# Kernel optimization log

Hardware: AMD Instinct MI355X
Metric: run time of the kernel (lower is better)

Reference implementation:

```python
import jax, jax.numpy as jnp
import numpy as np

H, L, N = 512, 2048, 64  # channels, seq len, SSM state size


def _make_dplr_hippo(n):
    # make_HiPPO / make_NPLR_HiPPO / make_DPLR_HiPPO from the source
    p0 = np.sqrt(1.0 + 2.0 * np.arange(n))
    A = p0[:, None] * p0[None, :]
    A = np.tril(A) - np.diag(np.arange(n))
    nhippo = -A
    P = np.sqrt(np.arange(n) + 0.5)
    B = np.sqrt(2.0 * np.arange(n) + 1.0)
    S = nhippo + P[:, None] * P[None, :]
    S_diag = np.diagonal(S)
    Lam_re = np.mean(S_diag) * np.ones_like(S_diag)
    Lam_im, V = jnp.linalg.eigh(jnp.asarray(S, jnp.complex64) * (-1j))
    Pc = V.conj().T @ jnp.asarray(P, jnp.complex64)
    Bc = V.conj().T @ jnp.asarray(B, jnp.complex64)
    return (jnp.asarray(Lam_re, jnp.float32), jnp.asarray(Lam_im, jnp.float32),
            Pc, Bc)


def setup_inputs() -> dict:
    key = jax.random.key(0)
    k_u, k_c, k_s = jax.random.split(key, 3)
    Lre, Lim, Pc, Bc = _make_dplr_hippo(N)
    tile = lambda v: jnp.tile(v[None, :], (H, 1)).astype(jnp.float32)  # (H,N)
    return {
        "u": jax.random.normal(k_u, (L, H), dtype=jnp.float32),
        "x0_re": jnp.zeros((N, H), jnp.float32),
        "x0_im": jnp.zeros((N, H), jnp.float32),
        "Lambda_re": tile(Lre),
        "Lambda_im": tile(Lim),
        "P_re": tile(Pc.real), "P_im": tile(Pc.imag),
        "B_re": tile(Bc.real), "B_im": tile(Bc.imag),
        "C": jax.random.normal(k_c, (H, N, 2), jnp.float32) * (0.5 ** 0.5),
        "D": jnp.ones((H, 1), jnp.float32),
        "log_step": jax.random.uniform(k_s, (H, 1), jnp.float32,
                                       minval=np.log(1e-3), maxval=np.log(1e-1)),
    }


def _discretize(Lam, P, B, Ct, step):
    # discrete_DPLR with Q = P (as in setup); per-channel, vmapped over H.
    n = Lam.shape[0]
    I = jnp.eye(n, dtype=jnp.complex64)
    A = jnp.diag(Lam) - P[:, None] * P.conj()[None, :]
    A0 = (2.0 / step) * I + A
    Dd = jnp.diag(1.0 / (2.0 / step - Lam))
    Qc = P.conj()[None, :]            # (1,N)
    P2 = P[:, None]                   # (N,1)
    A1 = Dd - (Dd @ P2) * (1.0 / (1.0 + Qc @ Dd @ P2)) * (Qc @ Dd)
    Ab = A1 @ A0                      # (N,N)
    Bb = 2.0 * (A1 @ B[:, None])[:, 0]
    AbL = jnp.linalg.matrix_power(Ab, L)
    Cb = (Ct[None, :] @ jnp.linalg.inv(I - AbL).conj()).conj()[0]
    return Ab, Bb, Cb


def _forward(u, x0_re, x0_im, Lambda_re, Lambda_im, P_re, P_im,
             B_re, B_im, C, D, log_step):
    Lam = jnp.clip(Lambda_re, None, -0.0001) + 1j * Lambda_im  # (H,N)
    Pc = P_re + 1j * P_im
    Bc = B_re + 1j * B_im
    Cc = C[..., 0] + 1j * C[..., 1]
    step = jnp.exp(log_step)[:, 0]                              # (H,)
    Ab, Bb, Cb = jax.vmap(_discretize)(Lam, Pc, Bc, Cc, step)   # (H,N,N),(H,N),(H,N)

    x0 = jnp.transpose(x0_re + 1j * x0_im)                      # (H,N) complex

    def body(x, u_t):  # x: (H,N) complex, u_t: (H,)
        x = jnp.einsum('hnm,hm->hn', Ab, x) + Bb * u_t[:, None]
        y = jnp.einsum('hn,hn->h', Cb, x)
        return x, y.real

    _, ys = jax.lax.scan(body, x0, u)                           # ys: (L,H)
    return ys + u * D[:, 0][None, :]                            # (L,H) float32


def reference(u, x0_re, x0_im, Lambda_re, Lambda_im, P_re, P_im,
              B_re, B_im, C, D, log_step):
    return _forward(u, x0_re, x0_im, Lambda_re, Lambda_im, P_re, P_im,
                    B_re, B_im, C, D, log_step)
```

## Files before the change

kernel.cpp:

```cpp
#include <hip/hip_runtime.h>

#define HH 512
#define LL 2048
#define NN 64
#define TT 64
#define CC 32
#define NLDA 68
#define SP 72

typedef __attribute__((ext_vector_type(8))) short bf16x8_t;
typedef __attribute__((ext_vector_type(4))) float floatx4;

__device__ __forceinline__ float2 cmul(float2 a, float2 b) {
    return make_float2(a.x * b.x - a.y * b.y, a.x * b.y + a.y * b.x);
}
__device__ __forceinline__ float2 crecip(float2 a) {
    float id = 1.0f / (a.x * a.x + a.y * a.y);
    return make_float2(a.x * id, -a.y * id);
}
template <int CTRL>
__device__ __forceinline__ float dpp_mov(float x) {
    return __int_as_float(__builtin_amdgcn_update_dpp(
        0, __float_as_int(x), CTRL, 0xf, 0xf, true));
}
__device__ __forceinline__ float wave_sum_bcast(float x) {
    x += dpp_mov<0x111>(x);
    x += dpp_mov<0x112>(x);
    x += dpp_mov<0x114>(x);
    x += dpp_mov<0x118>(x);
    x += dpp_mov<0x142>(x);
    x += dpp_mov<0x143>(x);
    return __int_as_float(__builtin_amdgcn_readlane(__float_as_int(x), 63));
}
__device__ __forceinline__ float rlane(float x, int i) {
    return __int_as_float(__builtin_amdgcn_readlane(__float_as_int(x), i));
}
__device__ __forceinline__ unsigned short f2bf(float f) {
    unsigned int u = __float_as_uint(f);
    u += 0x7FFFu + ((u >> 16) & 1u);
    return (unsigned short)(u >> 16);
}
__device__ __forceinline__ float bf2f(unsigned short s) {
    return __uint_as_float(((unsigned int)s) << 16);
}

__device__ __forceinline__ void closed_form(
    int h, int n,
    const float* __restrict__ Lre, const float* __restrict__ Lim,
    const float* __restrict__ Pre, const float* __restrict__ Pim,
    const float* __restrict__ Bre, const float* __restrict__ Bim,
    const float* __restrict__ logstep,
    float2& da, float2& DPv, float2& tv, float2& bb) {
    float step = expf(logstep[h]);
    float as = 2.0f / step;
    float lr = fminf(Lre[h * NN + n], -1e-4f);
    float li = Lim[h * NN + n];
    float2 a = make_float2(as + lr, li);
    float2 Dn = crecip(make_float2(as - lr, -li));
    float2 P = make_float2(Pre[h * NN + n], Pim[h * NN + n]);
    float2 Bv = make_float2(Bre[h * NN + n], Bim[h * NN + n]);
    float2 cP = make_float2(P.x, -P.y);
    float p2 = P.x * P.x + P.y * P.y;
    float2 rt = cmul(cmul(cP, Dn), Bv);
    float2 e = make_float2(wave_sum_bcast(Dn.x * p2), wave_sum_bcast(Dn.y * p2));
    float2 rv = make_float2(wave_sum_bcast(rt.x), wave_sum_bcast(rt.y));
    float2 cc = crecip(make_float2(1.0f + e.x, e.y));
    da = cmul(Dn, a);
    DPv = cmul(Dn, P);
    float2 tmp = cmul(cc, make_float2(da.x - e.x, da.y - e.y));
    tv = cmul(cP, make_float2(1.0f + tmp.x, tmp.y));
    float2 crv = cmul(cc, rv);
    float2 cd = cmul(crv, DPv);
    float2 db = cmul(Dn, Bv);
    bb = make_float2(2.0f * (db.x - cd.x), 2.0f * (db.y - cd.y));
}

__device__ __forceinline__ void pack_tiles(
    unsigned short* mRh, unsigned short* mRl,
    unsigned short* mIh, unsigned short* mIl,
    unsigned short* mTRh, unsigned short* mTRl,
    unsigned short* mTIh, unsigned short* mTIl,
    int w, int lm, int q, const float Cr[4][4], const float Ci[4][4]) {
    #pragma unroll
    for (int nt = 0; nt < 4; ++nt) {
        const int c = nt * 16 + lm;
        unsigned short hr[4], lr_[4], hi_[4], li_[4];
        #pragma unroll
        for (int reg = 0; reg < 4; ++reg) {
            const float xr = Cr[nt][reg], xi = Ci[nt][reg];
            hr[reg] = f2bf(xr); lr_[reg] = f2bf(xr - bf2f(hr[reg]));
            hi_[reg] = f2bf(xi); li_[reg] = f2bf(xi - bf2f(hi_[reg]));
            const int r = 16 * w + 4 * q + reg;
            mRh[r * SP + c] = hr[reg]; mRl[r * SP + c] = lr_[reg];
            mIh[r * SP + c] = hi_[reg]; mIl[r * SP + c] = li_[reg];
        }
        const int tb = c * SP + 16 * w + 4 * q;
        *(ushort4*)&mTRh[tb] = make_ushort4(hr[0], hr[1], hr[2], hr[3]);
        *(ushort4*)&mTRl[tb] = make_ushort4(lr_[0], lr_[1], lr_[2], lr_[3]);
        *(ushort4*)&mTIh[tb] = make_ushort4(hi_[0], hi_[1], hi_[2], hi_[3]);
        *(ushort4*)&mTIl[tb] = make_ushort4(li_[0], li_[1], li_[2], li_[3]);
    }
}

extern "C" __global__ void __launch_bounds__(256, 2)
k_fusedA(const float* __restrict__ Lre, const float* __restrict__ Lim,
         const float* __restrict__ Pre, const float* __restrict__ Pim,
         const float* __restrict__ Bre, const float* __restrict__ Bim,
         const float* __restrict__ Cmat, const float* __restrict__ logstep,
         const float* __restrict__ u,
         float2* __restrict__ wM, float2* __restrict__ wCb,
         float2* __restrict__ wP) {
    extern __shared__ __align__(16) char smem[];
    const int tid = threadIdx.x;

    if (blockIdx.x < HH) {
        const int h = blockIdx.x;
        unsigned short* mRh  = (unsigned short*)smem;
        unsigned short* mRl  = mRh + 64 * SP;
        unsigned short* mIh  = mRl + 64 * SP;
        unsigned short* mIl  = mIh + 64 * SP;
        unsigned short* mTRh = mIl + 64 * SP;
        unsigned short* mTRl = mTRh + 64 * SP;
        unsigned short* mTIh = mTRl + 64 * SP;
        unsigned short* mTIl = mTIh + 64 * SP;
        float* Nr = (float*)smem;
        float* Ni = Nr + 64 * NLDA;
        float2* sda  = (float2*)(smem + 73728);
        float2* sDP  = sda + NN;
        float2* st   = sDP + NN;
        float2* sBb  = st + NN;
        float2* srhs = sBb + NN;
        float2* sx   = srhs + NN;
        float2* pp   = sx + NN;

        const int w = tid >> 6;
        const int lane = tid & 63;
        const int lm = lane & 15, q = lane >> 4;

        if (tid < NN) {
            float2 da, DPv, tv, bb;
            closed_form(h, tid, Lre, Lim, Pre, Pim, Bre, Bim, logstep,
                        da, DPv, tv, bb);
            sda[tid] = da; sDP[tid] = DPv; st[tid] = tv; sBb[tid] = bb;
            srhs[tid] = make_float2(Cmat[h * NN * 2 + tid * 2],
                                    -Cmat[h * NN * 2 + tid * 2 + 1]);
        }
        __syncthreads();

        {
            float Cr[4][4], Ci[4][4];
            #pragma unroll
            for (int nt = 0; nt < 4; ++nt) {
                const int c = nt * 16 + lm;
                const float2 tc = st[c];
                #pragma unroll
                for (int reg = 0; reg < 4; ++reg) {
                    const int r = 16 * w + 4 * q + reg;
                    const float2 dp = sDP[r];
                    float vr = -(dp.x * tc.x - dp.y * tc.y);
                    float vi = -(dp.x * tc.y + dp.y * tc.x);
                    if (r == c) { vr += sda[r].x; vi += sda[r].y; }
                    Cr[nt][reg] = vr; Ci[nt][reg] = vi;
                }
            }
            pack_tiles(mRh, mRl, mIh, mIl, mTRh, mTRl, mTIh, mTIl,
                       w, lm, q, Cr, Ci);
        }
        __syncthreads();

        const int arow = (16 * w + lm) * SP + q * 8;
        for (int it = 0; it < 11; ++it) {
            floatx4 z4 = {0.f, 0.f, 0.f, 0.f};
            floatx4 aP[4] = {z4, z4, z4, z4};
            floatx4 aQ[4] = {z4, z4, z4, z4};
            floatx4 aC[4] = {z4, z4, z4, z4};
            for (int k2 = 0; k2 < 2; ++k2) {
                const int ao = arow + k2 * 32;
                const bf16x8_t ARh = *(const bf16x8_t*)&mRh[ao];
                const bf16x8_t ARl = *(const bf16x8_t*)&mRl[ao];
                const bf16x8_t AIh = *(const bf16x8_t*)&mIh[ao];
                const bf16x8_t AIl = *(const bf16x8_t*)&mIl[ao];
                bf16x8_t BRh[4], BRl[4], BIh[4], BIl[4];
                #pragma unroll
                for (int nt = 0; nt < 4; ++nt) {
                    const int bo = (nt * 16 + lm) * SP + k2 * 32 + q * 8;
                    BRh[nt] = *(const bf16x8_t*)&mTRh[bo];
                    BRl[nt] = *(const bf16x8_t*)&mTRl[bo];
                    BIh[nt] = *(const bf16x8_t*)&mTIh[bo];
                    BIl[nt] = *(const bf16x8_t*)&mTIl[bo];
                }
                #pragma unroll
                for (int nt = 0; nt < 4; ++nt) {
                    aP[nt] = __builtin_amdgcn_mfma_f32_16x16x32_bf16(ARh, BRh[nt], aP[nt], 0, 0, 0);
                    aP[nt] = __builtin_amdgcn_mfma_f32_16x16x32_bf16(ARh, BRl[nt], aP[nt], 0, 0, 0);
                    aP[nt] = __builtin_amdgcn_mfma_f32_16x16x32_bf16(ARl, BRh[nt], aP[nt], 0, 0, 0);
                    aQ[nt] = __builtin_amdgcn_mfma_f32_16x16x32_bf16(AIh, BIh[nt], aQ[nt], 0, 0, 0);
                    aQ[nt] = __builtin_amdgcn_mfma_f32_16x16x32_bf16(AIh, BIl[nt], aQ[nt], 0, 0, 0);
                    aQ[nt] = __builtin_amdgcn_mfma_f32_16x16x32_bf16(AIl, BIh[nt], aQ[nt], 0, 0, 0);
                    aC[nt] = __builtin_amdgcn_mfma_f32_16x16x32_bf16(ARh, BIh[nt], aC[nt], 0, 0, 0);
                    aC[nt] = __builtin_amdgcn_mfma_f32_16x16x32_bf16(ARh, BIl[nt], aC[nt], 0, 0, 0);
                    aC[nt] = __builtin_amdgcn_mfma_f32_16x16x32_bf16(ARl, BIh[nt], aC[nt], 0, 0, 0);
                    aC[nt] = __builtin_amdgcn_mfma_f32_16x16x32_bf16(AIh, BRh[nt], aC[nt], 0, 0, 0);
                    aC[nt] = __builtin_amdgcn_mfma_f32_16x16x32_bf16(AIh, BRl[nt], aC[nt], 0, 0, 0);
                    aC[nt] = __builtin_amdgcn_mfma_f32_16x16x32_bf16(AIl, BRh[nt], aC[nt], 0, 0, 0);
                }
            }
            __syncthreads();
            if (it < 10) {
                float Cr[4][4], Ci[4][4];
                #pragma unroll
                for (int nt = 0; nt < 4; ++nt)
                    #pragma unroll
                    for (int reg = 0; reg < 4; ++reg) {
                        Cr[nt][reg] = aP[nt][reg] - aQ[nt][reg];
                        Ci[nt][reg] = aC[nt][reg];
                    }
                pack_tiles(mRh, mRl, mIh, mIl, mTRh, mTRl, mTIh, mTIl,
                           w, lm, q, Cr, Ci);
                __syncthreads();
                if (it == 5) {
                    for (int idx = tid; idx < NN * NN; idx += 256) {
                        const int c = idx >> 6, k = idx & 63;
                        wM[h * NN * NN + idx] = make_float2(
                            bf2f(mTRh[c * SP + k]) + bf2f(mTRl[c * SP + k]),
                            bf2f(mTIh[c * SP + k]) + bf2f(mTIl[c * SP + k]));
                    }
                }
            } else {
                #pragma unroll
                for (int nt = 0; nt < 4; ++nt) {
                    const int c = nt * 16 + lm;
                    #pragma unroll
                    for (int reg = 0; reg < 4; ++reg) {
                        const int r = 16 * w + 4 * q + reg;
                        Nr[r * NLDA + c] = aP[nt][reg] - aQ[nt][reg];
                        Ni[r * NLDA + c] = aC[nt][reg];
                    }
                }
                __syncthreads();
            }
        }

        if (tid < NN) sx[tid] = srhs[tid];
        __syncthreads();
        for (int itn = 0; itn < 24; ++itn) {
            const int i = tid & 63, qq = tid >> 6;
            float pr = 0.0f, pi = 0.0f;
            #pragma unroll 4
            for (int jj = 0; jj < 16; ++jj) {
                const int j = qq * 16 + jj;
                const float nr = Nr[j * NLDA + i], ni = Ni[j * NLDA + i];
                const float2 xj = sx[j];
                pr += nr * xj.x - ni * xj.y;
                pi += nr * xj.y + ni * xj.x;
            }
            pp[qq * 64 + i] = make_float2(pr, pi);
            __syncthreads();
            if (tid < NN) {
                const float2 a0 = pp[tid], a1 = pp[64 + tid];
                const float2 a2 = pp[128 + tid], a3 = pp[192 + tid];
                sx[tid] = make_float2(
                    srhs[tid].x + a0.x + a1.x + a2.x + a3.x,
                    srhs[tid].y + a0.y + a1.y + a2.y + a3.y);
            }
            __syncthreads();
        }
        if (tid < NN) wCb[h * NN + tid] = sx[tid];
    } else {
        const int h = blockIdx.x - HH;
        float2* sG  = (float2*)smem;
        float*  su  = (float*)(smem + 32768);
        float2* sda = (float2*)(smem + 40960);
        float2* sDP = sda + NN;
        float2* st  = sDP + NN;
        float2* sBb = st + NN;

        const int wv = tid >> 6, lane = tid & 63;
        for (int idx = tid; idx < LL; idx += 256)
            su[idx] = u[idx * HH + h];
        if (tid < NN) {
            float2 da, DPv, tv, bb;
            closed_form(h, tid, Lre, Lim, Pre, Pim, Bre, Bim, logstep,
                        da, DPv, tv, bb);
            sda[tid] = da; sDP[tid] = DPv; st[tid] = tv; sBb[tid] = bb;
        }
        __syncthreads();

        if (tid < 64) {
            const float2 da = sda[lane], DP = sDP[lane], tt = st[lane];
            float Gr = sBb[lane].x, Gi = sBb[lane].y;
            for (int m = 0; m < TT; ++m) {
                sG[m * NN + lane] = make_float2(Gr, Gi);
                float c1 = tt.x * Gr - tt.y * Gi;
                float c2 = tt.x * Gi + tt.y * Gr;
                c1 += dpp_mov<0x111>(c1); c2 += dpp_mov<0x111>(c2);
                c1 += dpp_mov<0x112>(c1); c2 += dpp_mov<0x112>(c2);
                c1 += dpp_mov<0x114>(c1); c2 += dpp_mov<0x114>(c2);
                c1 += dpp_mov<0x118>(c1); c2 += dpp_mov<0x118>(c2);
                c1 += dpp_mov<0x142>(c1); c2 += dpp_mov<0x142>(c2);
                c1 += dpp_mov<0x143>(c1); c2 += dpp_mov<0x143>(c2);
                const float S1 = rlane(c1, 63);
                const float S2 = rlane(c2, 63);
                float nGr = da.x * Gr - da.y * Gi - (DP.x * S1 - DP.y * S2);
                float nGi = da.x * Gi + da.y * Gr - (DP.x * S2 + DP.y * S1);
                Gr = nGr; Gi = nGi;
            }
        }
        __syncthreads();

        float accr[8] = {}, acci[8] = {};
        for (int j = 0; j < TT; ++j) {
            const float2 g = sG[(TT - 1 - j) * NN + lane];
            #pragma unroll
            for (int qc = 0; qc < 8; ++qc) {
                const float uv = su[((wv * 8 + qc) << 6) + j];
                accr[qc] += g.x * uv; acci[qc] += g.y * uv;
            }
        }
        #pragma unroll
        for (int qc = 0; qc < 8; ++qc)
            wP[(h * CC + wv * 8 + qc) * NN + lane] = make_float2(accr[qc], acci[qc]);
    }
}

extern "C" __global__ void __launch_bounds__(256, 2)
k_fusedB(const float* __restrict__ Lre, const float* __restrict__ Lim,
         const float* __restrict__ Pre, const float* __restrict__ Pim,
         const float* __restrict__ Bre, const float* __restrict__ Bim,
         const float* __restrict__ logstep,
         const float* __restrict__ u, const float* __restrict__ Dvec,
         const float* __restrict__ x0_re, const float* __restrict__ x0_im,
         const float2* __restrict__ wM, const float2* __restrict__ wCb,
         const float2* __restrict__ wP, float* __restrict__ out) {
    extern __shared__ __align__(16) char smem[];
    float2* sM          = (float2*)smem;
    unsigned short* sVr = (unsigned short*)(smem + 32768);
    unsigned short* sVi = (unsigned short*)(smem + 41216);
    float2* sXs         = (float2*)(smem + 49664);
    float*  su          = (float*)(smem + 66048);
    float*  sK          = (float*)(smem + 74240);

    const int h = blockIdx.x;
    const int tid = threadIdx.x;
    const int wv = tid >> 6, lane = tid & 63;

    for (int idx = tid; idx < NN * NN; idx += 256)
        sM[idx] = wM[h * NN * NN + idx];
    for (int idx = tid; idx < LL; idx += 256)
        su[idx] = u[idx * HH + h];
    __syncthreads();

    if (wv == 0) {
        float2 da, DP, tt, Bb;
        closed_form(h, lane, Lre, Lim, Pre, Pim, Bre, Bim, logstep,
                    da, DP, tt, Bb);
        const float2 Cb = wCb[h * NN + lane];
        float Gr = Bb.x, Gi = Bb.y;
        float vr = Cb.x, vi = Cb.y;
        for (int m = 0; m < TT; ++m) {
            float ch[5];
            ch[0] = Cb.x * Gr - Cb.y * Gi;
            ch[1] = tt.x * Gr - tt.y * Gi;
            ch[2] = tt.x * Gi + tt.y * Gr;
            ch[3] = vr * DP.x - vi * DP.y;
            ch[4] = vr * DP.y + vi * DP.x;
            #pragma unroll
            for (int c = 0; c < 5; ++c) ch[c] += dpp_mov<0x111>(ch[c]);
            #pragma unroll
            for (int c = 0; c < 5; ++c) ch[c] += dpp_mov<0x112>(ch[c]);
            #pragma unroll
            for (int c = 0; c < 5; ++c) ch[c] += dpp_mov<0x114>(ch[c]);
            #pragma unroll
            for (int c = 0; c < 5; ++c) ch[c] += dpp_mov<0x118>(ch[c]);
            #pragma unroll
            for (int c = 0; c < 5; ++c) ch[c] += dpp_mov<0x142>(ch[c]);
            #pragma unroll
            for (int c = 0; c < 5; ++c) ch[c] += dpp_mov<0x143>(ch[c]);
            const float S0 = rlane(ch[0], 63);
            const float S1 = rlane(ch[1], 63);
            const float S2 = rlane(ch[2], 63);
            const float S3 = rlane(ch[3], 63);
            const float S4 = rlane(ch[4], 63);
            if (lane == 0) sK[m] = S0;
            float nGr = da.x * Gr - da.y * Gi - (DP.x * S1 - DP.y * S2);
            float nGi = da.x * Gi + da.y * Gr - (DP.x * S2 + DP.y * S1);
            Gr = nGr; Gi = nGi;
            float nvr = da.x * vr - da.y * vi - (S3 * tt.x - S4 * tt.y);
            float nvi = da.x * vi + da.y * vr - (S3 * tt.y + S4 * tt.x);
            vr = nvr; vi = nvi;
            sVr[lane * 66 + m] = f2bf(vr);
            sVi[lane * 66 + m] = f2bf(vi);
        }
    } else if (wv == 1) {
        float xr = x0_re[lane * HH + h], xi = x0_im[lane * HH + h];
        sXs[lane] = make_float2(xr, xi);
        float2 pe_next = wP[(h * CC + 0) * NN + lane];
        for (int c = 1; c < CC; ++c) {
            const float2 pe = pe_next;
            if (c < CC - 1) pe_next = wP[(h * CC + c) * NN + lane];
            float nr = 0.0f, ni = 0.0f;
            #pragma unroll 8
            for (int j = 0; j < NN; ++j) {
                const float xjr = rlane(xr, j);
                const float xji = rlane(xi, j);
                const float2 m = sM[j * NN + lane];
                nr += m.x * xjr - m.y * xji;
                ni += m.x * xji + m.y * xjr;
            }
            xr = nr + pe.x; xi = ni + pe.y;
            sXs[c * NN + lane] = make_float2(xr, xi);
        }
    }
    __syncthreads();

    const float Dh = Dvec[h];
    const int t = lane;
    float acc[8] = {};
    for (int s = 0; s < TT; ++s) {
        const int d = t - s;
        const float kv = (d >= 0) ? sK[d < 0 ? 0 : d] : 0.0f;
        #pragma unroll
        for (int qc = 0; qc < 8; ++qc)
            acc[qc] += kv * su[((wv * 8 + qc) << 6) + s];
    }
    for (int n = 0; n < NN; ++n) {
        const float vvr = bf2f(sVr[n * 66 + t]);
        const float vvi = bf2f(sVi[n * 66 + t]);
        #pragma unroll
        for (int qc = 0; qc < 8; ++qc) {
            const float2 xs = sXs[(wv * 8 + qc) * NN + n];
            acc[qc] += vvr * xs.x - vvi * xs.y;
        }
    }
    #pragma unroll
    for (int qc = 0; qc < 8; ++qc) {
        const int c = wv * 8 + qc;
        out[(c * TT + t) * HH + h] = acc[qc] + Dh * su[c * TT + t];
    }
}

extern "C" void kernel_launch(void* const* d_in, const int* in_sizes, int n_in,
                              void* d_out, int out_size, void* d_ws, size_t ws_size,
                              hipStream_t stream) {
    const float* u    = (const float*)d_in[0];
    const float* x0re = (const float*)d_in[1];
    const float* x0im = (const float*)d_in[2];
    const float* Lre  = (const float*)d_in[3];
    const float* Lim  = (const float*)d_in[4];
    const float* Pre  = (const float*)d_in[5];
    const float* Pim  = (const float*)d_in[6];
    const float* Bre  = (const float*)d_in[7];
    const float* Bim  = (const float*)d_in[8];
    const float* C    = (const float*)d_in[9];
    const float* Dv   = (const float*)d_in[10];
    const float* lst  = (const float*)d_in[11];

    float2* wM  = (float2*)d_ws;
    float2* wP  = wM + HH * NN * NN;
    float2* wCb = wP + HH * CC * NN;
    float* out = (float*)d_out;

    hipLaunchKernelGGL(k_fusedA, dim3(2 * HH), dim3(256), 78848, stream,
                       Lre, Lim, Pre, Pim, Bre, Bim, C, lst, u,
                       wM, wCb, wP);
    hipLaunchKernelGGL(k_fusedB, dim3(HH), dim3(256), 74496, stream,
                       Lre, Lim, Pre, Pim, Bre, Bim, lst, u, Dv,
                       x0re, x0im, wM, wCb, wP, out);
}
```

Baseline: 227.0 us.

## Use bf16 MFMA with split-precision state for chunk output and keep M in registers

The per-chunk V·x contraction in k_fusedB moves from scalar FMAs to bf16 16x16x32 MFMA, with the state split into high and low bf16 parts to keep accuracy. The 64x64 transition matrix now sits in registers of the recurrence wave instead of being staged in shared memory, and that loop uses four independent accumulators. The u load moves to the otherwise idle waves 2-3 so it overlaps the recurrence, and shared memory shrinks, which could allow more resident blocks. The costs are heavy register pressure in wave 1 (128 floats for M), an extra barrier, and the precision loss from bf16 inputs.

```diff
diff --git a/kernel.cpp b/kernel.cpp
--- a/kernel.cpp
+++ b/kernel.cpp
@@ -333,22 +333,20 @@
          const float2* __restrict__ wM, const float2* __restrict__ wCb,
          const float2* __restrict__ wP, float* __restrict__ out) {
     extern __shared__ __align__(16) char smem[];
-    float2* sM          = (float2*)smem;
-    unsigned short* sVr = (unsigned short*)(smem + 32768);
-    unsigned short* sVi = (unsigned short*)(smem + 41216);
-    float2* sXs         = (float2*)(smem + 49664);
-    float*  su          = (float*)(smem + 66048);
-    float*  sK          = (float*)(smem + 74240);
+    unsigned short* sVr  = (unsigned short*)smem;
+    unsigned short* sVi  = (unsigned short*)(smem + 9216);
+    unsigned short* sXrh = (unsigned short*)(smem + 18432);
+    unsigned short* sXrl = (unsigned short*)(smem + 23040);
+    unsigned short* sXih = (unsigned short*)(smem + 27648);
+    unsigned short* sXil = (unsigned short*)(smem + 32256);
+    float*          su   = (float*)(smem + 36864);
+    float*          sK   = (float*)(smem + 45056);
+    float*          y0   = (float*)(smem + 45312);
 
     const int h = blockIdx.x;
     const int tid = threadIdx.x;
     const int wv = tid >> 6, lane = tid & 63;
-
-    for (int idx = tid; idx < NN * NN; idx += 256)
-        sM[idx] = wM[h * NN * NN + idx];
-    for (int idx = tid; idx < LL; idx += 256)
-        su[idx] = u[idx * HH + h];
-    __syncthreads();
+    const int lm = lane & 15, q = lane >> 4;
 
     if (wv == 0) {
         float2 da, DP, tt, Bb;
@@ -388,54 +386,96 @@
             float nvr = da.x * vr - da.y * vi - (S3 * tt.x - S4 * tt.y);
             float nvi = da.x * vi + da.y * vr - (S3 * tt.y + S4 * tt.x);
             vr = nvr; vi = nvi;
-            sVr[lane * 66 + m] = f2bf(vr);
-            sVi[lane * 66 + m] = f2bf(vi);
+            sVr[m * SP + lane] = f2bf(vr);
+            sVi[m * SP + lane] = f2bf(-vi);
         }
     } else if (wv == 1) {
+        float Mr[NN], Mi[NN];
+        const float2* __restrict__ wMh = wM + h * NN * NN;
+        #pragma unroll
+        for (int j = 0; j < NN; ++j) {
+            const float2 v = wMh[j * NN + lane];
+            Mr[j] = v.x; Mi[j] = v.y;
+        }
         float xr = x0_re[lane * HH + h], xi = x0_im[lane * HH + h];
-        sXs[lane] = make_float2(xr, xi);
+        {
+            const unsigned short hr = f2bf(xr), hi_ = f2bf(xi);
+            sXrh[lane] = hr;  sXrl[lane] = f2bf(xr - bf2f(hr));
+            sXih[lane] = hi_; sXil[lane] = f2bf(xi - bf2f(hi_));
+        }
         float2 pe_next = wP[(h * CC + 0) * NN + lane];
         for (int c = 1; c < CC; ++c) {
             const float2 pe = pe_next;
             if (c < CC - 1) pe_next = wP[(h * CC + c) * NN + lane];
-            float nr = 0.0f, ni = 0.0f;
-            #pragma unroll 8
+            float ar[4] = {0.f, 0.f, 0.f, 0.f};
+            float ai[4] = {0.f, 0.f, 0.f, 0.f};
+            #pragma unroll
             for (int j = 0; j < NN; ++j) {
                 const float xjr = rlane(xr, j);
                 const float xji = rlane(xi, j);
-                const float2 m = sM[j * NN + lane];
-                nr += m.x * xjr - m.y * xji;
-                ni += m.x * xji + m.y * xjr;
-            }
-            xr = nr + pe.x; xi = ni + pe.y;
-            sXs[c * NN + lane] = make_float2(xr, xi);
-        }
+                ar[j & 3] = fmaf(Mr[j], xjr, ar[j & 3]);
+                ar[j & 3] = fmaf(-Mi[j], xji, ar[j & 3]);
+                ai[j & 3] = fmaf(Mr[j], xji, ai[j & 3]);
+                ai[j & 3] = fmaf(Mi[j], xjr, ai[j & 3]);
+            }
+            xr = ((ar[0] + ar[1]) + (ar[2] + ar[3])) + pe.x;
+            xi = ((ai[0] + ai[1]) + (ai[2] + ai[3])) + pe.y;
+            const unsigned short hr = f2bf(xr), hi_ = f2bf(xi);
+            sXrh[c * SP + lane] = hr;  sXrl[c * SP + lane] = f2bf(xr - bf2f(hr));
+            sXih[c * SP + lane] = hi_; sXil[c * SP + lane] = f2bf(xi - bf2f(hi_));
+        }
+    } else {
+        for (int idx = tid - 128; idx < LL; idx += 128)
+            su[idx] = u[idx * HH + h];
     }
     __syncthreads();
 
-    const float Dh = Dvec[h];
-    const int t = lane;
-    float acc[8] = {};
-    for (int s = 0; s < TT; ++s) {
-        const int d = t - s;
-        const float kv = (d >= 0) ? sK[d < 0 ? 0 : d] : 0.0f;
-        #pragma unroll
-        for (int qc = 0; qc < 8; ++qc)
-            acc[qc] += kv * su[((wv * 8 + qc) << 6) + s];
-    }
-    for (int n = 0; n < NN; ++n) {
-        const float vvr = bf2f(sVr[n * 66 + t]);
-        const float vvi = bf2f(sVi[n * 66 + t]);
+    {
+        const float Dh = Dvec[h];
+        float acc[8] = {};
+        for (int s = 0; s < TT; ++s) {
+            const int d = lane - s;
+            const float kv = (d >= 0) ? sK[d < 0 ? 0 : d] : 0.0f;
+            #pragma unroll
+            for (int qc = 0; qc < 8; ++qc)
+                acc[qc] += kv * su[((wv * 8 + qc) << 6) + s];
+        }
         #pragma unroll
         for (int qc = 0; qc < 8; ++qc) {
-            const float2 xs = sXs[(wv * 8 + qc) * NN + n];
-            acc[qc] += vvr * xs.x - vvi * xs.y;
+            const int c = wv * 8 + qc;
+            y0[c * 65 + lane] = acc[qc] + Dh * su[c * 64 + lane];
+        }
+    }
+    __syncthreads();
+
+    floatx4 z4 = {0.f, 0.f, 0.f, 0.f};
+    floatx4 acc2[2] = {z4, z4};
+    #pragma unroll
+    for (int k2 = 0; k2 < 2; ++k2) {
+        const int ak = (16 * wv + lm) * SP + k2 * 32 + q * 8;
+        const bf16x8_t aVr = *(const bf16x8_t*)&sVr[ak];
+        const bf16x8_t aVi = *(const bf16x8_t*)&sVi[ak];
+        #pragma unroll
+        for (int nt = 0; nt < 2; ++nt) {
+            const int bk = (nt * 16 + lm) * SP + k2 * 32 + q * 8;
+            const bf16x8_t bRh = *(const bf16x8_t*)&sXrh[bk];
+            const bf16x8_t bRl = *(const bf16x8_t*)&sXrl[bk];
+            const bf16x8_t bIh = *(const bf16x8_t*)&sXih[bk];
+            const bf16x8_t bIl = *(const bf16x8_t*)&sXil[bk];
+            acc2[nt] = __builtin_amdgcn_mfma_f32_16x16x32_bf16(aVr, bRh, acc2[nt], 0, 0, 0);
+            acc2[nt] = __builtin_amdgcn_mfma_f32_16x16x32_bf16(aVr, bRl, acc2[nt], 0, 0, 0);
+            acc2[nt] = __builtin_amdgcn_mfma_f32_16x16x32_bf16(aVi, bIh, acc2[nt], 0, 0, 0);
+            acc2[nt] = __builtin_amdgcn_mfma_f32_16x16x32_bf16(aVi, bIl, acc2[nt], 0, 0, 0);
         }
     }
     #pragma unroll
-    for (int qc = 0; qc < 8; ++qc) {
-        const int c = wv * 8 + qc;
-        out[(c * TT + t) * HH + h] = acc[qc] + Dh * su[c * TT + t];
+    for (int nt = 0; nt < 2; ++nt) {
+        #pragma unroll
+        for (int reg = 0; reg < 4; ++reg) {
+            const int c = nt * 16 + lm;
+            const int t = 16 * wv + 4 * q + reg;
+            out[(c * TT + t) * HH + h] = acc2[nt][reg] + y0[c * 65 + t];
+        }
     }
 }
 
@@ -463,7 +503,7 @@
     hipLaunchKernelGGL(k_fusedA, dim3(2 * HH), dim3(256), 78848, stream,
                        Lre, Lim, Pre, Pim, Bre, Bim, C, lst, u,
                        wM, wCb, wP);
-    hipLaunchKernelGGL(k_fusedB, dim3(HH), dim3(256), 74496, stream,
+    hipLaunchKernelGGL(k_fusedB, dim3(HH), dim3(256), 53632, stream,
                        Lre, Lim, Pre, Pim, Bre, Bim, lst, u, Dv,
                        x0re, x0im, wM, wCb, wP, out);
 }
```

Measured after the change: 227.1 us. No clear change (+0.1%).
